# Kernel tuning notes

Hardware: AMD Instinct MI355X
Metric: run time of the kernel (lower is better)

Reference implementation:

```python
import jax, jax.numpy as jnp
import numpy as np

N, M, D, DV = 16384, 16384, 8, 16
BLOCK = 2048  # row tile size; kernel block is [BLOCK, M], never materialize full [N, M]


def setup_inputs() -> dict:
    key = jax.random.key(0)
    k1, k2, k3, k4 = jax.random.split(key, 4)
    ls = jax.random.uniform(k1, (D,), dtype=jnp.float32)          # per-dim lengthscale weights (positive)
    x = jax.random.normal(k2, (N, D), dtype=jnp.float32)
    y = jax.random.normal(k3, (M, D), dtype=jnp.float32)
    b = jax.random.normal(k4, (M, DV), dtype=jnp.float32)
    return {"ls": ls, "x": x, "y": y, "b": b}


def reference(ls, x, y, b):
    # Matern nu=2.5 kernel-weighted reduction:
    #   d2_ij = sum_d ls_d * (x_id - y_jd)^2
    #   K_ij  = (1 + c1*sqrt(d2) + c2*d2) * exp(-c1*sqrt(d2))   (c1=sqrt(5), c2=sqrt(5/3), as in the torch module)
    #   out_i = sum_j K_ij * b_j   -- computed in row tiles (KeOps-style online reduction)
    c1 = jnp.sqrt(jnp.asarray(5.0, x.dtype))
    c2 = jnp.sqrt(jnp.asarray(5.0 / 3.0, x.dtype))

    def row_block(xi):  # xi: [BLOCK, D]
        diff = xi[:, None, :] - y[None, :, :]                 # [BLOCK, M, D]
        d2 = jnp.einsum('d,bmd->bm', ls, diff * diff)         # [BLOCK, M]
        r = jnp.sqrt(d2)
        k = (1.0 + c1 * r + c2 * d2) * jnp.exp(-c1 * r)       # [BLOCK, M]
        return k @ b                                          # [BLOCK, DV]

    xb = x.reshape(-1, BLOCK, x.shape[1])                     # [N/BLOCK, BLOCK, D]
    out = jax.lax.map(row_block, xb)                          # [N/BLOCK, BLOCK, DV]
    return out.reshape(-1, b.shape[1])                        # [N, DV]
```

## Files before the change

kernel.cpp:

```cpp
#include <hip/hip_runtime.h>
#include <stdint.h>

#define NN 16384
#define MM 16384
#define DD 8
#define DV 16
#define WAVES 4
#define MT 2
#define ROWS_WAVE (MT * 16)
#define ROWS_BLK (WAVES * ROWS_WAVE)
#define JSPLIT 16
#define JCHUNK (MM / JSPLIT)
#define J32 (JCHUNK / 32)

typedef short bf8 __attribute__((ext_vector_type(8)));
typedef float f32x4 __attribute__((ext_vector_type(4)));

__device__ __forceinline__ unsigned short f2bf(float f) {
    union { float f; uint32_t u; } c; c.f = f;
    uint32_t u = c.u + 0x7FFF + ((c.u >> 16) & 1);
    return (unsigned short)(u >> 16);
}
__device__ __forceinline__ float bf2f(unsigned short h) {
    union { float f; uint32_t u; } c; c.u = ((uint32_t)h) << 16;
    return c.f;
}

#define BF16_ONE ((short)0x3F80)

__global__ __launch_bounds__(64) void prep_frags(const float* __restrict__ ls,
                                                 const float* __restrict__ y,
                                                 const float* __restrict__ b,
                                                 bf8* __restrict__ ytbl,
                                                 bf8* __restrict__ btbl) {
    const int tile = blockIdx.x;
    const int lane = threadIdx.x;
    const int n = lane & 15, quad = lane >> 4;

    float lsv[DD];
#pragma unroll
    for (int d = 0; d < DD; ++d) lsv[d] = ls[d];

    const float* yr = y + (size_t)(tile * 16 + n) * DD;
    float syv = 0.f;
    unsigned short yh[DD], yl[DD];
#pragma unroll
    for (int d = 0; d < DD; ++d) {
        float yv = yr[d];
        syv = fmaf(lsv[d] * yv, yv, syv);
        yh[d] = f2bf(yv);
        yl[d] = f2bf(yv - bf2f(yh[d]));
    }

    bf8 fr;
    if (quad < 3) {
#pragma unroll
        for (int d = 0; d < DD; ++d) {
            unsigned short base = (quad == 2) ? yl[d] : yh[d];
            fr[d] = (short)f2bf(-2.f * bf2f(base));
        }
    } else {
        unsigned short sh = f2bf(syv);
        unsigned short sl = f2bf(syv - bf2f(sh));
        fr[0] = (short)sh;
        fr[1] = (short)sl;
        fr[2] = BF16_ONE;
        fr[3] = BF16_ONE;
        fr[4] = 0; fr[5] = 0; fr[6] = 0; fr[7] = 0;
    }
    ytbl[tile * 64 + lane] = fr;

    if (tile < MM / 32) {
        bf8 bfr;
#pragma unroll
        for (int s = 0; s < 8; ++s) {
            float bv = b[(size_t)(tile * 32 + quad * 8 + s) * DV + n];
            bfr[s] = (short)f2bf(bv);
        }
        btbl[tile * 64 + lane] = bfr;
    }
}

__global__ __launch_bounds__(256, 8) void matern_mfma(const float* __restrict__ ls,
                                                      const float* __restrict__ x,
                                                      const bf8* __restrict__ ytbl,
                                                      const bf8* __restrict__ btbl,
                                                      float* __restrict__ out) {
    const int t = threadIdx.x;
    const int lane = t & 63, wave = t >> 6;
    const int n = lane & 15, quad = lane >> 4;
    const int waverow = blockIdx.x * ROWS_BLK + wave * ROWS_WAVE;

    __shared__ __attribute__((aligned(16))) unsigned short klds[WAVES][MT][16][40];

    float lsv[DD];
#pragma unroll
    for (int d = 0; d < DD; ++d) lsv[d] = ls[d];

    bf8 afrag[MT];
#pragma unroll
    for (int mt = 0; mt < MT; ++mt) {
        const float* xr = x + (size_t)(waverow + mt * 16 + n) * DD;
        float sx = 0.f;
        unsigned short xh[DD], xl[DD];
#pragma unroll
        for (int d = 0; d < DD; ++d) {
            float xv = xr[d];
            float xlsv = lsv[d] * xv;
            sx = fmaf(xlsv, xv, sx);
            xh[d] = f2bf(xlsv);
            xl[d] = f2bf(xlsv - bf2f(xh[d]));
        }
        bf8 fr;
        if (quad == 3) {
            unsigned short sh = f2bf(sx);
            unsigned short sl = f2bf(sx - bf2f(sh));
            fr[0] = BF16_ONE;
            fr[1] = BF16_ONE;
            fr[2] = (short)sh;
            fr[3] = (short)sl;
            fr[4] = 0; fr[5] = 0; fr[6] = 0; fr[7] = 0;
        } else {
#pragma unroll
            for (int d = 0; d < DD; ++d)
                fr[d] = (short)((quad == 1) ? xl[d] : xh[d]);
        }
        afrag[mt] = fr;
    }

    const float c1 = 2.23606797749979f;
    const float c2 = 1.2909944487358056f;
    const float c3 = -3.2259641843312987f;

    f32x4 acc[MT];
#pragma unroll
    for (int mt = 0; mt < MT; ++mt) acc[mt] = (f32x4){0.f, 0.f, 0.f, 0.f};

    const int tile16base = blockIdx.y * (JCHUNK / 16);
    const int tile32base = blockIdx.y * (JCHUNK / 32);

#pragma unroll 1
    for (int it = 0; it < J32; ++it) {
        const int tl0 = tile16base + it * 2;
        bf8 yA = ytbl[(size_t)tl0 * 64 + lane];
        bf8 yB = ytbl[(size_t)(tl0 + 1) * 64 + lane];
        bf8 bb = btbl[(size_t)(tile32base + it) * 64 + lane];

#pragma unroll
        for (int mt = 0; mt < MT; ++mt) {
            f32x4 z = (f32x4){0.f, 0.f, 0.f, 0.f};
            f32x4 s0 = __builtin_amdgcn_mfma_f32_16x16x32_bf16(afrag[mt], yA, z, 0, 0, 0);
            f32x4 s1 = __builtin_amdgcn_mfma_f32_16x16x32_bf16(afrag[mt], yB, z, 0, 0, 0);
#pragma unroll
            for (int s = 0; s < 4; ++s) {
                float d20 = fmaxf(s0[s], 0.f);
                float d21 = fmaxf(s1[s], 0.f);
                float r0 = __builtin_amdgcn_sqrtf(d20);
                float r1 = __builtin_amdgcn_sqrtf(d21);
                float e0 = __builtin_amdgcn_exp2f(c3 * r0);
                float e1 = __builtin_amdgcn_exp2f(c3 * r1);
                float k0 = fmaf(c2, d20, fmaf(c1, r0, 1.f)) * e0;
                float k1 = fmaf(c2, d21, fmaf(c1, r1, 1.f)) * e1;
#if __has_builtin(__builtin_amdgcn_cvt_pk_bf16_f32)
                typedef __bf16 bf2v __attribute__((ext_vector_type(2)));
                bf2v pk = __builtin_amdgcn_cvt_pk_bf16_f32(k0, k1);
                union { bf2v v; unsigned short u[2]; } cv; cv.v = pk;
                klds[wave][mt][quad * 4 + s][n] = cv.u[0];
                klds[wave][mt][quad * 4 + s][n + 16] = cv.u[1];
#else
                klds[wave][mt][quad * 4 + s][n] =
                    (unsigned short)((__float_as_uint(k0) + 0x8000u) >> 16);
                klds[wave][mt][quad * 4 + s][n + 16] =
                    (unsigned short)((__float_as_uint(k1) + 0x8000u) >> 16);
#endif
            }
        }
#pragma unroll
        for (int mt = 0; mt < MT; ++mt) {
            const bf8* kp = (const bf8*)&klds[wave][mt][n][quad * 8];
            acc[mt] = __builtin_amdgcn_mfma_f32_16x16x32_bf16(*kp, bb, acc[mt], 0, 0, 0);
        }
    }

#pragma unroll
    for (int mt = 0; mt < MT; ++mt)
#pragma unroll
        for (int s = 0; s < 4; ++s) {
            const int row = waverow + mt * 16 + quad * 4 + s;
            atomicAdd(out + (size_t)row * DV + n, acc[mt][s]);
        }
}

extern "C" void kernel_launch(void* const* d_in, const int* in_sizes, int n_in,
                              void* d_out, int out_size, void* d_ws, size_t ws_size,
                              hipStream_t stream) {
    const float* ls = (const float*)d_in[0];
    const float* x  = (const float*)d_in[1];
    const float* y  = (const float*)d_in[2];
    const float* b  = (const float*)d_in[3];
    float* out = (float*)d_out;

    char* ws = (char*)d_ws;
    bf8* ytbl = (bf8*)ws;
    bf8* btbl = (bf8*)(ws + (1 << 20));

    hipMemsetAsync(d_out, 0, (size_t)out_size * sizeof(float), stream);
    prep_frags<<<MM / 16, 64, 0, stream>>>(ls, y, b, ytbl, btbl);
    matern_mfma<<<dim3(NN / ROWS_BLK, JSPLIT), 256, 0, stream>>>(ls, x, ytbl, btbl, out);
}
```

Baseline: 151.7 us.

## Fold output zeroing into prep kernel, double J split, and trim Matern math

Drops the separate memset and zeroes the output inside a widened prep kernel that uses 4 waves per block and float4 loads of y. It also doubles the J split of the main kernel to give it more blocks, at the cost of twice as many output atomics. The Matern evaluation folds the exp2 scale into the sqrt argument and swaps the max-with-zero clamp for fabs, saving a multiply per element. A leftover float4 pointer for b is computed but never used.

```diff
diff --git a/kernel.cpp b/kernel.cpp
--- a/kernel.cpp
+++ b/kernel.cpp
@@ -9,7 +9,7 @@
 #define MT 2
 #define ROWS_WAVE (MT * 16)
 #define ROWS_BLK (WAVES * ROWS_WAVE)
-#define JSPLIT 16
+#define JSPLIT 32
 #define JCHUNK (MM / JSPLIT)
 #define J32 (JCHUNK / 32)
 
@@ -28,28 +28,33 @@
 
 #define BF16_ONE ((short)0x3F80)
 
-__global__ __launch_bounds__(64) void prep_frags(const float* __restrict__ ls,
-                                                 const float* __restrict__ y,
-                                                 const float* __restrict__ b,
-                                                 bf8* __restrict__ ytbl,
-                                                 bf8* __restrict__ btbl) {
-    const int tile = blockIdx.x;
-    const int lane = threadIdx.x;
+__global__ __launch_bounds__(256) void prep_frags(const float* __restrict__ ls,
+                                                  const float* __restrict__ y,
+                                                  const float* __restrict__ b,
+                                                  bf8* __restrict__ ytbl,
+                                                  bf8* __restrict__ btbl,
+                                                  float4* __restrict__ outz) {
+    const int tile = blockIdx.x * 4 + (threadIdx.x >> 6);
+    const int lane = threadIdx.x & 63;
     const int n = lane & 15, quad = lane >> 4;
 
+    outz[blockIdx.x * 256 + threadIdx.x] = make_float4(0.f, 0.f, 0.f, 0.f);
+
     float lsv[DD];
 #pragma unroll
     for (int d = 0; d < DD; ++d) lsv[d] = ls[d];
 
-    const float* yr = y + (size_t)(tile * 16 + n) * DD;
+    const float4* yr4 = (const float4*)(y + (size_t)(tile * 16 + n) * DD);
+    float4 ya = yr4[0], yb = yr4[1];
+    float yv[DD] = {ya.x, ya.y, ya.z, ya.w, yb.x, yb.y, yb.z, yb.w};
+
     float syv = 0.f;
     unsigned short yh[DD], yl[DD];
 #pragma unroll
     for (int d = 0; d < DD; ++d) {
-        float yv = yr[d];
-        syv = fmaf(lsv[d] * yv, yv, syv);
-        yh[d] = f2bf(yv);
-        yl[d] = f2bf(yv - bf2f(yh[d]));
+        syv = fmaf(lsv[d] * yv[d], yv[d], syv);
+        yh[d] = f2bf(yv[d]);
+        yl[d] = f2bf(yv[d] - bf2f(yh[d]));
     }
 
     bf8 fr;
@@ -72,11 +77,13 @@
 
     if (tile < MM / 32) {
         bf8 bfr;
+        const float4* br4 = (const float4*)(b + (size_t)(tile * 32) * DV);
 #pragma unroll
         for (int s = 0; s < 8; ++s) {
             float bv = b[(size_t)(tile * 32 + quad * 8 + s) * DV + n];
             bfr[s] = (short)f2bf(bv);
         }
+        (void)br4;
         btbl[tile * 64 + lane] = bfr;
     }
 }
@@ -128,9 +135,9 @@
         afrag[mt] = fr;
     }
 
-    const float c1 = 2.23606797749979f;
-    const float c2 = 1.2909944487358056f;
-    const float c3 = -3.2259641843312987f;
+    const float c3sq = 10.406922f;
+    const float ln2  = 0.6931471805599453f;
+    const float c2   = 1.2909944487358056f;
 
     f32x4 acc[MT];
 #pragma unroll
@@ -153,14 +160,14 @@
             f32x4 s1 = __builtin_amdgcn_mfma_f32_16x16x32_bf16(afrag[mt], yB, z, 0, 0, 0);
 #pragma unroll
             for (int s = 0; s < 4; ++s) {
-                float d20 = fmaxf(s0[s], 0.f);
-                float d21 = fmaxf(s1[s], 0.f);
-                float r0 = __builtin_amdgcn_sqrtf(d20);
-                float r1 = __builtin_amdgcn_sqrtf(d21);
-                float e0 = __builtin_amdgcn_exp2f(c3 * r0);
-                float e1 = __builtin_amdgcn_exp2f(c3 * r1);
-                float k0 = fmaf(c2, d20, fmaf(c1, r0, 1.f)) * e0;
-                float k1 = fmaf(c2, d21, fmaf(c1, r1, 1.f)) * e1;
+                float a0 = __builtin_fabsf(s0[s]);
+                float a1 = __builtin_fabsf(s1[s]);
+                float t0 = __builtin_amdgcn_sqrtf(c3sq * a0);
+                float t1 = __builtin_amdgcn_sqrtf(c3sq * a1);
+                float e0 = __builtin_amdgcn_exp2f(-t0);
+                float e1 = __builtin_amdgcn_exp2f(-t1);
+                float k0 = fmaf(c2, a0, fmaf(ln2, t0, 1.f)) * e0;
+                float k1 = fmaf(c2, a1, fmaf(ln2, t1, 1.f)) * e1;
 #if __has_builtin(__builtin_amdgcn_cvt_pk_bf16_f32)
                 typedef __bf16 bf2v __attribute__((ext_vector_type(2)));
                 bf2v pk = __builtin_amdgcn_cvt_pk_bf16_f32(k0, k1);
@@ -204,7 +211,6 @@
     bf8* ytbl = (bf8*)ws;
     bf8* btbl = (bf8*)(ws + (1 << 20));
 
-    hipMemsetAsync(d_out, 0, (size_t)out_size * sizeof(float), stream);
-    prep_frags<<<MM / 16, 64, 0, stream>>>(ls, y, b, ytbl, btbl);
+    prep_frags<<<MM / 64, 256, 0, stream>>>(ls, y, b, ytbl, btbl, (float4*)out);
     matern_mfma<<<dim3(NN / ROWS_BLK, JSPLIT), 256, 0, stream>>>(ls, x, ytbl, btbl, out);
 }
```

Result: faster. 138.1 us (-9.0%).
